# Performance work log

Measured on AMD Instinct MI355X. Metric: run time of the kernel, lower is better.

The kernel has to match this reference:

```python
import jax, jax.numpy as jnp
import numpy as np

B, S, HID = 1, 1024, 4096
NH, NKV, HD = 32, 8, 128
GROUPS = NH // NKV
THETA = 10000.0
SPAR = 0.5          # sparse_aggression (layer_idx > 0)
MIN_IDX = 4         # min_sparse_index: always-kept sink tokens
NEG = jnp.float32(-1e30)


def setup_inputs() -> dict:
    key = jax.random.key(0)
    k0, k1, k2, k3, k4 = jax.random.split(key, 5)
    sc = 0.02
    return {
        "hidden_states": jax.random.normal(k0, (B, S, HID), jnp.float32),
        "position_ids": jnp.arange(S, dtype=jnp.int32)[None, :],
        "Wq": jax.random.normal(k1, (NH * HD, HID), jnp.float32) * sc,
        "Wk": jax.random.normal(k2, (NKV * HD, HID), jnp.float32) * sc,
        "Wv": jax.random.normal(k3, (NKV * HD, HID), jnp.float32) * sc,
        "Wo": jax.random.normal(k4, (HID, NH * HD), jnp.float32) * sc,
    }


def _rotate_half(x):
    h = x.shape[-1] // 2
    return jnp.concatenate([-x[..., h:], x[..., :h]], axis=-1)


def _rope_cos_sin(position_ids):
    inv_freq = 1.0 / (THETA ** (jnp.arange(0, HD, 2, dtype=jnp.float32) / HD))
    freqs = position_ids.astype(jnp.float32)[..., None] * inv_freq  # [B,S,HD/2]
    emb = jnp.concatenate([freqs, freqs], axis=-1)                  # [B,S,HD]
    return jnp.cos(emb)[:, None], jnp.sin(emb)[:, None]             # [B,1,S,HD]


def reference(hidden_states, position_ids, Wq, Wk, Wv, Wo):
    b, s, _ = hidden_states.shape
    # QKV projections (nn.Linear: x @ W.T)
    q = (hidden_states @ Wq.T).reshape(b, s, NH, HD).transpose(0, 2, 1, 3)
    k = (hidden_states @ Wk.T).reshape(b, s, NKV, HD).transpose(0, 2, 1, 3)
    v = (hidden_states @ Wv.T).reshape(b, s, NKV, HD).transpose(0, 2, 1, 3)
    # RoPE
    cos, sin = _rope_cos_sin(position_ids)
    q = q * cos + _rotate_half(q) * sin
    k = k * cos + _rotate_half(k) * sin
    # repeat_kv (GQA expansion)
    k = jnp.repeat(k, GROUPS, axis=1)
    v = jnp.repeat(v, GROUPS, axis=1)
    # causal additive mask [1,1,S,S]
    causal = jnp.where(jnp.triu(jnp.ones((s, s), bool), 1), NEG, jnp.float32(0))[None, None]
    scale = 1.0 / np.sqrt(HD)
    scores = jnp.einsum('bhqd,bhkd->bhqk', q, k) * scale
    # oracle importance: softmax of (softmaxed) masked attention (no_grad in original)
    oracle = jax.nn.softmax((scores + causal).astype(jnp.float32), axis=-1)
    importance = jax.nn.softmax(oracle, axis=-1)
    importance = jax.lax.stop_gradient(importance)
    # descending sort -> rank of each key for each query
    sorted_idx = jnp.argsort(-importance, axis=-1)          # [B,H,S,S]
    ranks = jnp.argsort(sorted_idx, axis=-1)                # inverse perm
    # per-query token budget: keep ceil-ish top-k proportional to row length
    k_per_row = jnp.maximum((SPAR * (jnp.arange(s) + 1)).astype(jnp.int32), 1)
    key_idx = jnp.arange(s)
    kept = (ranks < k_per_row[None, None, :, None]) | (key_idx[None, None, None, :] < MIN_IDX)
    sparse_mask = jnp.where(kept, jnp.float32(0), NEG)
    # sparse attention
    attn = scores + sparse_mask + causal
    probs = jax.nn.softmax(attn.astype(jnp.float32), axis=-1).astype(v.dtype)
    out = jnp.einsum('bhqk,bhkd->bhqd', probs, v)           # [B,H,S,HD]
    out = out.transpose(0, 2, 1, 3).reshape(b, s, NH * HD)
    return out @ Wo.T
```

## Files before the change

### kernel.cpp

```cpp
#include <hip/hip_runtime.h>
#include <hip/hip_bf16.h>

#define S_LEN 1024
#define HID   4096
#define NH    32
#define NKV   8
#define HD    128
#define MIN_IDX 4
#define AO_COLS 4096
#define HEAD_STRIDE 131072

typedef __attribute__((ext_vector_type(8))) short short8;
typedef __attribute__((ext_vector_type(4))) float f32x4;

__device__ __forceinline__ unsigned short f2bf(float f) {
  union { float f; unsigned u; } v; v.f = f;
  unsigned r = v.u + 0x7FFFu + ((v.u >> 16) & 1u);
  return (unsigned short)(r >> 16);
}
__device__ __forceinline__ float bf2f(unsigned short h) {
  union { unsigned u; float f; } v; v.u = ((unsigned)h) << 16;
  return v.f;
}
__device__ __forceinline__ unsigned pk2(float a, float b) {
  union { __hip_bfloat162 h; unsigned u; } c;
  c.h = __float22bfloat162_rn(make_float2(a, b));
  return c.u;
}
__device__ __forceinline__ short8 pack8(float4 a, float4 b) {
  union { short8 s; unsigned u[4]; } r;
  r.u[0] = pk2(a.x, a.y); r.u[1] = pk2(a.z, a.w);
  r.u[2] = pk2(b.x, b.y); r.u[3] = pk2(b.z, b.w);
  return r.s;
}
__device__ __forceinline__ unsigned ordf(float f) {
  union { float f; int i; } v; v.f = f;
  return (unsigned)(v.i ^ ((v.i >> 31) | 0x80000000));
}
__device__ __forceinline__ float iordf(unsigned u) {
  union { int i; float f; } v;
  v.i = (u & 0x80000000u) ? (int)(u ^ 0x80000000u) : (int)~u;
  return v.f;
}
__device__ __forceinline__ float wave_sum_f(float v) {
  #pragma unroll
  for (int m = 32; m >= 1; m >>= 1) v += __shfl_xor(v, m);
  return v;
}
__device__ __forceinline__ unsigned wave_max_u(unsigned v) {
  #pragma unroll
  for (int m = 32; m >= 1; m >>= 1) { unsigned o = __shfl_xor(v, m); v = o > v ? o : v; }
  return v;
}
__device__ __forceinline__ void wave_lds_fence() {
  __builtin_amdgcn_s_waitcnt(0xC07F);
  __builtin_amdgcn_wave_barrier();
}
__device__ __forceinline__ void gload_lds16(const unsigned short* g, unsigned short* l) {
  auto gp = (const __attribute__((address_space(1))) unsigned*)g;
  auto lp = (__attribute__((address_space(3))) unsigned*)(unsigned)(unsigned long long)l;
  __builtin_amdgcn_global_load_lds(gp, lp, 16, 0, 0);
}

__global__ __launch_bounds__(256) void cvt_k(
    const float* __restrict__ src, unsigned short* __restrict__ dst)
{
  const size_t i = ((size_t)blockIdx.x * 256 + threadIdx.x) * 8;
  float4 a = *(const float4*)(src + i);
  float4 b = *(const float4*)(src + i + 4);
  *(short8*)(dst + i) = pack8(a, b);
}

__global__ __launch_bounds__(256) void cvt4_k(
    const float* __restrict__ s0, const float* __restrict__ s1,
    const float* __restrict__ s2, const float* __restrict__ s3,
    unsigned short* __restrict__ d0, unsigned short* __restrict__ d1)
{
  const int b = blockIdx.x;
  const float* src; unsigned short* dst; int rb;
  if (b < 2048)       { src = s0; dst = d0;            rb = b; }
  else if (b < 10240) { src = s1; dst = d1;            rb = b - 2048; }
  else if (b < 12288) { src = s2; dst = d1 + 16777216; rb = b - 10240; }
  else                { src = s3; dst = d1 + 20971520; rb = b - 12288; }
  const size_t i = ((size_t)rb * 256 + threadIdx.x) * 8;
  float4 a = *(const float4*)(src + i);
  float4 c = *(const float4*)(src + i + 4);
  *(short8*)(dst + i) = pack8(a, c);
}

__global__ __launch_bounds__(256) void gemm_qkv_k(
    const unsigned short* __restrict__ Xb, const unsigned short* __restrict__ Wb,
    unsigned short* __restrict__ Qraw, unsigned short* __restrict__ Kraw,
    unsigned short* __restrict__ Vt)
{
  __shared__ unsigned short As[3][128 * 32];
  __shared__ unsigned short Bs[3][128 * 32];
  const int nt = blockIdx.x;
  const int n0 = nt * 128;
  const int m0 = blockIdx.y * 128;
  const int t = threadIdx.x, w = t >> 6, lane = t & 63;
  const int wm = w >> 1, wn = w & 1;
  const int mcol = lane & 15, quad = lane >> 4;
  const int lrow = lane >> 2, lcol = (lane & 3) * 8;

  const unsigned short* Ag = Xb + (size_t)m0 * HID;
  const unsigned short* Bg = Wb + (size_t)n0 * HID;

  f32x4 acc[4][4];
  #pragma unroll
  for (int i = 0; i < 4; i++)
    #pragma unroll
    for (int j = 0; j < 4; j++) acc[i][j] = (f32x4){0.f, 0.f, 0.f, 0.f};

  constexpr int NT = HID / 32;
  #define STAGE_QKV(buf, k0)                                                  \
    { const int c0 = w * 2, c1 = w * 2 + 1;                                   \
      gload_lds16(Ag + (size_t)(c0*16 + lrow) * HID + (k0) + lcol, &As[buf][c0 * 512]); \
      gload_lds16(Bg + (size_t)(c0*16 + lrow) * HID + (k0) + lcol, &Bs[buf][c0 * 512]); \
      gload_lds16(Ag + (size_t)(c1*16 + lrow) * HID + (k0) + lcol, &As[buf][c1 * 512]); \
      gload_lds16(Bg + (size_t)(c1*16 + lrow) * HID + (k0) + lcol, &Bs[buf][c1 * 512]); }

  STAGE_QKV(0, 0)
  STAGE_QKV(1, 32)
  asm volatile("s_waitcnt vmcnt(4)" ::: "memory");
  __builtin_amdgcn_s_barrier();
  __builtin_amdgcn_sched_barrier(0);

  int cur = 0, stg = 2;
  for (int kt = 0; kt < NT; ++kt) {
    if (kt + 2 < NT) STAGE_QKV(stg, (kt + 2) * 32)
    short8 af[4], bf[4];
    #pragma unroll
    for (int i = 0; i < 4; i++) af[i] = *(const short8*)&As[cur][(wm*64 + i*16 + mcol)*32 + quad*8];
    #pragma unroll
    for (int j = 0; j < 4; j++) bf[j] = *(const short8*)&Bs[cur][(wn*64 + j*16 + mcol)*32 + quad*8];
    #pragma unroll
    for (int i = 0; i < 4; i++)
      #pragma unroll
      for (int j = 0; j < 4; j++)
        acc[i][j] = __builtin_amdgcn_mfma_f32_16x16x32_bf16(af[i], bf[j], acc[i][j], 0, 0, 0);
    if (kt + 2 < NT) { asm volatile("s_waitcnt vmcnt(4)" ::: "memory"); }
    else             { asm volatile("s_waitcnt vmcnt(0)" ::: "memory"); }
    __builtin_amdgcn_s_barrier();
    __builtin_amdgcn_sched_barrier(0);
    cur = (cur == 2) ? 0 : cur + 1;
    stg = (stg == 2) ? 0 : stg + 1;
  }

  if (nt < 40) {
    unsigned short* dst = (nt < 32) ? (Qraw + (size_t)nt * HEAD_STRIDE)
                                    : (Kraw + (size_t)(nt - 32) * HEAD_STRIDE);
    #pragma unroll
    for (int i = 0; i < 4; i++) {
      const int rb = m0 + wm*64 + i*16 + quad*4;
      #pragma unroll
      for (int j = 0; j < 4; j++) {
        const int d = wn*64 + j*16 + mcol;
        #pragma unroll
        for (int r = 0; r < 4; r++)
          dst[(size_t)(rb + r) * HD + d] = f2bf(acc[i][j][r]);
      }
    }
  } else {
    unsigned short* dst = Vt + (size_t)(nt - 40) * HEAD_STRIDE;
    #pragma unroll
    for (int i = 0; i < 4; i++) {
      const int rb = m0 + wm*64 + i*16 + quad*4;
      #pragma unroll
      for (int j = 0; j < 4; j++) {
        const int d = wn*64 + j*16 + mcol;
        ushort4 v4;
        v4.x = f2bf(acc[i][j][0]); v4.y = f2bf(acc[i][j][1]);
        v4.z = f2bf(acc[i][j][2]); v4.w = f2bf(acc[i][j][3]);
        *(ushort4*)(dst + (size_t)d * S_LEN + rb) = v4;
      }
    }
  }
}

__global__ __launch_bounds__(256) void rope_qk_k(
    const int* __restrict__ pos_ids,
    unsigned short* __restrict__ Qraw, unsigned short* __restrict__ Kraw)
{
  const int w = threadIdx.x >> 6, lane = threadIdx.x & 63;
  const int gw = blockIdx.x * 4 + w;
  const int hidx = gw >> 10;
  const int s = gw & 1023;
  const float pos = (float)pos_ids[s];
  const float invf = exp2f((float)lane * -0.20762050593045f);
  float sn, cs;
  sincosf(pos * invf, &sn, &cs);
  unsigned short* base = (hidx < NH)
      ? (Qraw + (size_t)hidx * HEAD_STRIDE + (size_t)s * HD)
      : (Kraw + (size_t)(hidx - NH) * HEAD_STRIDE + (size_t)s * HD);
  const float x0 = bf2f(base[lane]), x1 = bf2f(base[lane + 64]);
  base[lane]      = f2bf(x0 * cs - x1 * sn);
  base[lane + 64] = f2bf(x1 * cs + x0 * sn);
}

#define SROW 1042
#define PSTR 2084

#define PROC_ROW(UARR, RR, LL, PRE, PM, KRM, TTT)                             \
  {                                                                           \
    const int r_ = (RR);                                                      \
    const int L_ = (LL);                                                      \
    unsigned btau = (PRE);                                                    \
    unsigned bmsk = (PM);                                                     \
    int kr = (KRM);                                                           \
    int tt = (TTT);                                                           \
    const int bs = (bmsk == 0u) ? 31 : (__builtin_ctz(bmsk) - 1);             \
    _Pragma("unroll 1")                                                       \
    for (int b = bs; b >= 0; --b) {                                           \
      if (tt <= kr) break;                                                    \
      const unsigned bit = 1u << b;                                           \
      const unsigned am = bmsk | bit;                                         \
      const unsigned test = btau | bit;                                       \
      int cnt = 0;                                                            \
      _Pragma("unroll")                                                       \
      for (int c = 0; c < NC; c++) {                                          \
        const int j = c * 64 + lane;                                          \
        cnt += (int)__popcll(__ballot(j < L_ && ((UARR)[c] & am) == test));   \
      }                                                                       \
      if (cnt >= kr) { btau = test; tt = cnt; }                               \
      else           { kr -= cnt; tt -= cnt; }                                \
      bmsk = am;                                                              \
    }                                                                         \
    unsigned um = 0;                                                          \
    _Pragma("unroll")                                                         \
    for (int c = 0; c < NC; c++) {                                            \
      const int j = c * 64 + lane;                                            \
      if (j < L_ && (UARR)[c] > um) um = (UARR)[c];                           \
    }                                                                         \
    const float mx = iordf(wave_max_u(um));                                   \
    float ssum = 0.f;                                                         \
    int tiebase = 0;                                                          \
    _Pragma("unroll")                                                         \
    for (int c = 0; c < NC; c++) {                                            \
      const int j = c * 64 + lane;                                            \
      const unsigned u = (UARR)[c];                                           \
      const unsigned umv = u & bmsk;                                          \
      const bool eq = (j < L_) && (umv == btau);                              \
      const unsigned long long bal = __ballot(eq);                            \
      const int trank = tiebase + (int)__popcll(bal & lmlt);                  \
      tiebase += (int)__popcll(bal);                                          \
      const bool kept = (j < L_) &&                                           \
          ((umv > btau) || (eq && trank < kr) || (j < MIN_IDX));              \
      const float e = kept ? __expf(iordf(u) - mx) : 0.f;                     \
      Pl[r_][c*64 + lane] = f2bf(e);                                          \
      ssum += e;                                                              \
    }                                                                         \
    ssum = wave_sum_f(ssum);                                                  \
    if (lane == 0) rowinv[r_] = 1.f / fmaxf(ssum, 1e-30f);                    \
  }

template<int KT>
__device__ __forceinline__ void attn_body(
    const unsigned short* __restrict__ Qb, const unsigned short* __restrict__ Kh,
    const unsigned short* __restrict__ Vh, unsigned short* __restrict__ AO,
    float (*S)[SROW], unsigned (*hist)[256], float* rowinv,
    int q0, int h, int w, int lane, int mcol, int quad)
{
  constexpr int NC = 2 * KT;
  const float scale = 0.08838834764831845f;
  unsigned short (*Pl)[PSTR] = (unsigned short (*)[PSTR])&S[0][0];
  const int wk = w & 3, wp = w >> 2;

  short8 aq[4];
  {
    const unsigned short* qrow = Qb + ((size_t)h * S_LEN + q0 + mcol) * HD + quad * 8;
    #pragma unroll
    for (int kk = 0; kk < 4; kk++) aq[kk] = *(const short8*)(qrow + kk * 32);
  }

  #pragma unroll
  for (int kt = wp; kt < KT; kt += 2) {
    short8 bfr[2][4];
    #pragma unroll
    for (int g2 = 0; g2 < 2; g2++) {
      const int key = kt * 128 + (wk * 2 + g2) * 16 + mcol;
      const unsigned short* krow = Kh + (size_t)key * HD + quad * 8;
      #pragma unroll
      for (int kk = 0; kk < 4; kk++) bfr[g2][kk] = *(const short8*)(krow + kk * 32);
    }
    f32x4 d4[2];
    d4[0] = (f32x4){0.f,0.f,0.f,0.f}; d4[1] = (f32x4){0.f,0.f,0.f,0.f};
    #pragma unroll
    for (int g2 = 0; g2 < 2; g2++)
      #pragma unroll
      for (int kk = 0; kk < 4; kk++)
        d4[g2] = __builtin_amdgcn_mfma_f32_16x16x32_bf16(aq[kk], bfr[g2][kk], d4[g2], 0, 0, 0);
    #pragma unroll
    for (int g2 = 0; g2 < 2; g2++) {
      const int ckey = kt * 128 + (wk * 2 + g2) * 16 + mcol;
      #pragma unroll
      for (int r = 0; r < 4; r++) S[quad*4 + r][ckey] = d4[g2][r] * scale;
    }
  }
  __syncthreads();

  const unsigned long long lmlt = (1ull << lane) - 1ull;
  const int rep = lane & 3;
  {
    const int ra = w * 2, rbn = ra + 1;
    const int L0 = q0 + ra + 1, L1 = q0 + rbn + 1;
    unsigned u0[NC], u1[NC];
    #pragma unroll
    for (int c = 0; c < NC; c++) {
      u0[c] = ordf(S[ra][c*64 + lane]);
      u1[c] = ordf(S[rbn][c*64 + lane]);
    }
    int ks0 = L0 >> 1; if (ks0 < 1) ks0 = 1;
    int ks1 = L1 >> 1; if (ks1 < 1) ks1 = 1;
    int krem0 = ks0, tot0 = L0, krem1 = ks1, tot1 = L1;
    unsigned pre0 = 0u, pre1 = 0u, pm0 = 0u, pm1 = 0u;

    #pragma unroll
    for (int pass = 0; pass < 3; pass++) {
      const int shift = 26 - pass * 6;
      const bool a0 = tot0 > krem0, a1 = tot1 > krem1;
      if (!a0 && !a1) continue;
      { uint4 z = {0u, 0u, 0u, 0u}; *(uint4*)&hist[w][lane * 4] = z; }
      wave_lds_fence();
      #pragma unroll
      for (int c = 0; c < NC; c++) {
        const int j = c * 64 + lane;
        if (a0 && j < L0 && (u0[c] & pm0) == pre0)
          atomicAdd(&hist[w][((u0[c] >> shift) & 63) * 4 + rep], 1u);
        if (a1 && j < L1 && (u1[c] & pm1) == pre1)
          atomicAdd(&hist[w][((u1[c] >> shift) & 63) * 4 + rep], 1u << 16);
      }
      wave_lds_fence();
      const uint4 cv = *(const uint4*)&hist[w][(63 - lane) * 4];
      const unsigned cnt2 = cv.x + cv.y + cv.z + cv.w;
      unsigned x = cnt2;
      #pragma unroll
      for (int d2 = 1; d2 < 64; d2 <<= 1) { unsigned y = __shfl_up(x, d2); if (lane >= d2) x += y; }
      const unsigned runp = x - cnt2;
      if (a0) {
        const int run = (int)(runp & 0xFFFFu);
        const int cn  = (int)(cnt2 & 0xFFFFu);
        const bool hit = (run < krem0) && (run + cn >= krem0);
        unsigned packv = hit ? (((unsigned)(63 - lane) << 22) |
                                ((unsigned)run << 11) | (unsigned)cn) : 0u;
        const unsigned long long bal = __ballot(hit);
        const int srcl = __ffsll(bal) - 1;
        const unsigned res = __shfl(packv, srcl);
        krem0 -= (int)((res >> 11) & 0x7FF);
        tot0 = (int)(res & 0x7FF);
        pre0 |= ((unsigned)(res >> 22)) << shift;
        pm0 |= 63u << shift;
      }
      if (a1) {
        const int run = (int)(runp >> 16);
        const int cn  = (int)(cnt2 >> 16);
        const bool hit = (run < krem1) && (run + cn >= krem1);
        unsigned packv = hit ? (((unsigned)(63 - lane) << 22) |
                                ((unsigned)run << 11) | (unsigned)cn) : 0u;
        const unsigned long long bal = __ballot(hit);
        const int srcl = __ffsll(bal) - 1;
        const unsigned res = __shfl(packv, srcl);
        krem1 -= (int)((res >> 11) & 0x7FF);
        tot1 = (int)(res & 0x7FF);
        pre1 |= ((unsigned)(res >> 22)) << shift;
        pm1 |= 63u << shift;
      }
    }
    PROC_ROW(u0, ra,  L0, pre0, pm0, krem0, tot0)
    PROC_ROW(u1, rbn, L1, pre1, pm1, krem1, tot1)
  }
  __syncthreads();

  f32x4 opv = (f32x4){0.f,0.f,0.f,0.f};
  const int d = w * 16 + mcol;
  #pragma unroll
  for (int kt = 0; kt < KT; kt++) {
    #pragma unroll
    for (int kb = 0; kb < 4; kb++) {
      short8 af = *(const short8*)&Pl[mcol][kt*128 + kb*32 + quad*8];
      short8 bfr = *(const short8*)(Vh + (size_t)d * S_LEN + kt*128 + kb*32 + quad*8);
      opv = __builtin_amdgcn_mfma_f32_16x16x32_bf16(af, bfr, opv, 0, 0, 0);
    }
  }
  {
    const int col = h * HD + d;
    #pragma unroll
    for (int r2 = 0; r2 < 4; r2++) {
      const int row = q0 + quad*4 + r2;
      AO[(size_t)row * AO_COLS + col] = f2bf(opv[r2] * rowinv[quad*4 + r2]);
    }
  }
}

__global__ __launch_bounds__(512, 4) void attn_k(
    const unsigned short* __restrict__ Qb, const unsigned short* __restrict__ Kb,
    const unsigned short* __restrict__ Vt, unsigned short* __restrict__ AO)
{
  __shared__ float S[16][SROW];
  __shared__ unsigned hist[8][256];
  __shared__ float rowinv[16];
  const int rb = (int)gridDim.x - 1 - (int)blockIdx.x;
  const int h = blockIdx.y;
  const int kvh = h >> 2;
  const int q0 = rb * 16;
  const int kt_max = (rb >> 3) + 1;
  const int t = threadIdx.x, w = t >> 6, lane = t & 63;
  const int mcol = lane & 15, quad = lane >> 4;
  const unsigned short* Kh = Kb + (size_t)kvh * HEAD_STRIDE;
  const unsigned short* Vh = Vt + (size_t)kvh * HEAD_STRIDE;

  switch (kt_max) {
    case 1: attn_body<1>(Qb, Kh, Vh, AO, S, hist, rowinv, q0, h, w, lane, mcol, quad); break;
    case 2: attn_body<2>(Qb, Kh, Vh, AO, S, hist, rowinv, q0, h, w, lane, mcol, quad); break;
    case 3: attn_body<3>(Qb, Kh, Vh, AO, S, hist, rowinv, q0, h, w, lane, mcol, quad); break;
    case 4: attn_body<4>(Qb, Kh, Vh, AO, S, hist, rowinv, q0, h, w, lane, mcol, quad); break;
    case 5: attn_body<5>(Qb, Kh, Vh, AO, S, hist, rowinv, q0, h, w, lane, mcol, quad); break;
    case 6: attn_body<6>(Qb, Kh, Vh, AO, S, hist, rowinv, q0, h, w, lane, mcol, quad); break;
    case 7: attn_body<7>(Qb, Kh, Vh, AO, S, hist, rowinv, q0, h, w, lane, mcol, quad); break;
    default: attn_body<8>(Qb, Kh, Vh, AO, S, hist, rowinv, q0, h, w, lane, mcol, quad); break;
  }
}

__global__ __launch_bounds__(256) void gemm_out_k(
    const unsigned short* __restrict__ A, const unsigned short* __restrict__ Wob,
    float* __restrict__ Out)
{
  __shared__ unsigned short As[3][128 * 32];
  __shared__ unsigned short Bs[3][128 * 32];
  const int n0 = blockIdx.x * 128;
  const int m0 = blockIdx.y * 128;
  const int t = threadIdx.x, w = t >> 6, lane = t & 63;
  const int wm = w >> 1, wn = w & 1;
  const int mcol = lane & 15, quad = lane >> 4;
  const int lrow = lane >> 2, lcol = (lane & 3) * 8;

  const unsigned short* Ag = A   + (size_t)m0 * AO_COLS;
  const unsigned short* Bg = Wob + (size_t)n0 * AO_COLS;

  f32x4 acc[4][4];
  #pragma unroll
  for (int i = 0; i < 4; i++)
    #pragma unroll
    for (int j = 0; j < 4; j++) acc[i][j] = (f32x4){0.f, 0.f, 0.f, 0.f};

  constexpr int NT = AO_COLS / 32;
  #define STAGE_OUT(buf, k0)                                                  \
    { const int c0 = w * 2, c1 = w * 2 + 1;                                   \
      gload_lds16(Ag + (size_t)(c0*16 + lrow) * AO_COLS + (k0) + lcol, &As[buf][c0 * 512]); \
      gload_lds16(Bg + (size_t)(c0*16 + lrow) * AO_COLS + (k0) + lcol, &Bs[buf][c0 * 512]); \
      gload_lds16(Ag + (size_t)(c1*16 + lrow) * AO_COLS + (k0) + lcol, &As[buf][c1 * 512]); \
      gload_lds16(Bg + (size_t)(c1*16 + lrow) * AO_COLS + (k0) + lcol, &Bs[buf][c1 * 512]); }

  STAGE_OUT(0, 0)
  STAGE_OUT(1, 32)
  asm volatile("s_waitcnt vmcnt(4)" ::: "memory");
  __builtin_amdgcn_s_barrier();
  __builtin_amdgcn_sched_barrier(0);

  int cur = 0, stg = 2;
  for (int kt = 0; kt < NT; ++kt) {
    if (kt + 2 < NT) STAGE_OUT(stg, (kt + 2) * 32)
    short8 af[4], bf[4];
    #pragma unroll
    for (int i = 0; i < 4; i++) af[i] = *(const short8*)&As[cur][(wm*64 + i*16 + mcol)*32 + quad*8];
    #pragma unroll
    for (int j = 0; j < 4; j++) bf[j] = *(const short8*)&Bs[cur][(wn*64 + j*16 + mcol)*32 + quad*8];
    #pragma unroll
    for (int i = 0; i < 4; i++)
      #pragma unroll
      for (int j = 0; j < 4; j++)
        acc[i][j] = __builtin_amdgcn_mfma_f32_16x16x32_bf16(af[i], bf[j], acc[i][j], 0, 0, 0);
    if (kt + 2 < NT) { asm volatile("s_waitcnt vmcnt(4)" ::: "memory"); }
    else             { asm volatile("s_waitcnt vmcnt(0)" ::: "memory"); }
    __builtin_amdgcn_s_barrier();
    __builtin_amdgcn_sched_barrier(0);
    cur = (cur == 2) ? 0 : cur + 1;
    stg = (stg == 2) ? 0 : stg + 1;
  }

  #pragma unroll
  for (int i = 0; i < 4; i++) {
    const int rb = m0 + wm*64 + i*16 + quad*4;
    #pragma unroll
    for (int j = 0; j < 4; j++) {
      const int col = n0 + wn*64 + j*16 + mcol;
      #pragma unroll
      for (int r = 0; r < 4; r++)
        Out[(size_t)(rb + r) * HID + col] = acc[i][j][r];
    }
  }
}

extern "C" void kernel_launch(void* const* d_in, const int* in_sizes, int n_in,
                              void* d_out, int out_size, void* d_ws, size_t ws_size,
                              hipStream_t stream) {
  (void)in_sizes; (void)n_in; (void)out_size; (void)ws_size;
  const float* X   = (const float*)d_in[0];
  const int*   pos = (const int*)d_in[1];
  const float* Wq  = (const float*)d_in[2];
  const float* Wk  = (const float*)d_in[3];
  const float* Wv  = (const float*)d_in[4];
  const float* Wo  = (const float*)d_in[5];
  float* out = (float*)d_out;

  char* ws = (char*)d_ws;
  unsigned short* Qraw  = (unsigned short*)ws;
  unsigned short* Kraw  = (unsigned short*)(ws + 8388608);
  unsigned short* Vt    = (unsigned short*)(ws + 10485760);
  unsigned short* AO    = (unsigned short*)(ws + 12582912);
  unsigned short* Xb    = (unsigned short*)(ws + 20971520);
  unsigned short* Wqkvb = (unsigned short*)(ws + 29360128);
  unsigned short* Wob   = Wqkvb;

  cvt4_k<<<dim3(14336), dim3(256), 0, stream>>>(X, Wq, Wk, Wv, Xb, Wqkvb);

  gemm_qkv_k<<<dim3(48, 8),  dim3(256), 0, stream>>>(Xb, Wqkvb, Qraw, Kraw, Vt);
  rope_qk_k <<<dim3(10240),  dim3(256), 0, stream>>>(pos, Qraw, Kraw);

  cvt_k<<<dim3(8192), dim3(256), 0, stream>>>(Wo, Wob);

  attn_k    <<<dim3(64, 32), dim3(512), 0, stream>>>(Qraw, Kraw, Vt, AO);
  gemm_out_k<<<dim3(32, 8),  dim3(256), 0, stream>>>(AO, Wob, out);
}
```

Baseline: 462.7 us.

## Halve GEMM N-tiles for better CU fill and add tie-free fast path in top-k

Both the QKV and output-projection GEMMs move from 128x128 to 128x64 tiles, doubling the block count, with per-kernel launch-bound occupancy hints and fewer B-tile loads per stage. The QKV kernel now treats Q and K as one contiguous buffer, so the separate K pointer is dropped from it and from RoPE. The attention top-k masking gains a fast path that skips tie ranking with ballots whenever the threshold bucket holds no more keys than are still needed. The aim is better occupancy across the GPU's compute units for the GEMMs and fewer wave-wide reductions in the sparse softmax. The cost is less data reuse per tile in the GEMMs.

```diff
diff --git a/kernel.cpp b/kernel.cpp
--- a/kernel.cpp
+++ b/kernel.cpp
@@ -88,15 +88,14 @@
   *(short8*)(dst + i) = pack8(a, c);
 }
 
-__global__ __launch_bounds__(256) void gemm_qkv_k(
+__global__ __launch_bounds__(256, 3) void gemm_qkv_k(
     const unsigned short* __restrict__ Xb, const unsigned short* __restrict__ Wb,
-    unsigned short* __restrict__ Qraw, unsigned short* __restrict__ Kraw,
-    unsigned short* __restrict__ Vt)
+    unsigned short* __restrict__ Qraw, unsigned short* __restrict__ Vt)
 {
   __shared__ unsigned short As[3][128 * 32];
-  __shared__ unsigned short Bs[3][128 * 32];
+  __shared__ unsigned short Bs[3][64 * 32];
   const int nt = blockIdx.x;
-  const int n0 = nt * 128;
+  const int n0 = nt * 64;
   const int m0 = blockIdx.y * 128;
   const int t = threadIdx.x, w = t >> 6, lane = t & 63;
   const int wm = w >> 1, wn = w & 1;
@@ -106,40 +105,39 @@
   const unsigned short* Ag = Xb + (size_t)m0 * HID;
   const unsigned short* Bg = Wb + (size_t)n0 * HID;
 
-  f32x4 acc[4][4];
+  f32x4 acc[4][2];
   #pragma unroll
   for (int i = 0; i < 4; i++)
     #pragma unroll
-    for (int j = 0; j < 4; j++) acc[i][j] = (f32x4){0.f, 0.f, 0.f, 0.f};
+    for (int j = 0; j < 2; j++) acc[i][j] = (f32x4){0.f, 0.f, 0.f, 0.f};
 
   constexpr int NT = HID / 32;
   #define STAGE_QKV(buf, k0)                                                  \
     { const int c0 = w * 2, c1 = w * 2 + 1;                                   \
       gload_lds16(Ag + (size_t)(c0*16 + lrow) * HID + (k0) + lcol, &As[buf][c0 * 512]); \
-      gload_lds16(Bg + (size_t)(c0*16 + lrow) * HID + (k0) + lcol, &Bs[buf][c0 * 512]); \
       gload_lds16(Ag + (size_t)(c1*16 + lrow) * HID + (k0) + lcol, &As[buf][c1 * 512]); \
-      gload_lds16(Bg + (size_t)(c1*16 + lrow) * HID + (k0) + lcol, &Bs[buf][c1 * 512]); }
+      gload_lds16(Bg + (size_t)(w*16 + lrow) * HID + (k0) + lcol, &Bs[buf][w * 512]); }
 
   STAGE_QKV(0, 0)
   STAGE_QKV(1, 32)
-  asm volatile("s_waitcnt vmcnt(4)" ::: "memory");
+  asm volatile("s_waitcnt vmcnt(3)" ::: "memory");
   __builtin_amdgcn_s_barrier();
   __builtin_amdgcn_sched_barrier(0);
 
   int cur = 0, stg = 2;
   for (int kt = 0; kt < NT; ++kt) {
     if (kt + 2 < NT) STAGE_QKV(stg, (kt + 2) * 32)
-    short8 af[4], bf[4];
+    short8 af[4], bfr[2];
     #pragma unroll
     for (int i = 0; i < 4; i++) af[i] = *(const short8*)&As[cur][(wm*64 + i*16 + mcol)*32 + quad*8];
     #pragma unroll
-    for (int j = 0; j < 4; j++) bf[j] = *(const short8*)&Bs[cur][(wn*64 + j*16 + mcol)*32 + quad*8];
+    for (int j = 0; j < 2; j++) bfr[j] = *(const short8*)&Bs[cur][(wn*32 + j*16 + mcol)*32 + quad*8];
     #pragma unroll
     for (int i = 0; i < 4; i++)
       #pragma unroll
-      for (int j = 0; j < 4; j++)
-        acc[i][j] = __builtin_amdgcn_mfma_f32_16x16x32_bf16(af[i], bf[j], acc[i][j], 0, 0, 0);
-    if (kt + 2 < NT) { asm volatile("s_waitcnt vmcnt(4)" ::: "memory"); }
+      for (int j = 0; j < 2; j++)
+        acc[i][j] = __builtin_amdgcn_mfma_f32_16x16x32_bf16(af[i], bfr[j], acc[i][j], 0, 0, 0);
+    if (kt + 2 < NT) { asm volatile("s_waitcnt vmcnt(3)" ::: "memory"); }
     else             { asm volatile("s_waitcnt vmcnt(0)" ::: "memory"); }
     __builtin_amdgcn_s_barrier();
     __builtin_amdgcn_sched_barrier(0);
@@ -147,28 +145,30 @@
     stg = (stg == 2) ? 0 : stg + 1;
   }
 
-  if (nt < 40) {
-    unsigned short* dst = (nt < 32) ? (Qraw + (size_t)nt * HEAD_STRIDE)
-                                    : (Kraw + (size_t)(nt - 32) * HEAD_STRIDE);
+  if (nt < 80) {
+    unsigned short* dst = Qraw + (size_t)(n0 >> 7) * HEAD_STRIDE;
+    const int cb = n0 & 127;
     #pragma unroll
     for (int i = 0; i < 4; i++) {
       const int rb = m0 + wm*64 + i*16 + quad*4;
       #pragma unroll
-      for (int j = 0; j < 4; j++) {
-        const int d = wn*64 + j*16 + mcol;
+      for (int j = 0; j < 2; j++) {
+        const int d = cb + wn*32 + j*16 + mcol;
         #pragma unroll
         for (int r = 0; r < 4; r++)
           dst[(size_t)(rb + r) * HD + d] = f2bf(acc[i][j][r]);
       }
     }
   } else {
-    unsigned short* dst = Vt + (size_t)(nt - 40) * HEAD_STRIDE;
+    const int v0 = n0 - 5120;
+    unsigned short* dst = Vt + (size_t)(v0 >> 7) * HEAD_STRIDE;
+    const int cb = v0 & 127;
     #pragma unroll
     for (int i = 0; i < 4; i++) {
       const int rb = m0 + wm*64 + i*16 + quad*4;
       #pragma unroll
-      for (int j = 0; j < 4; j++) {
-        const int d = wn*64 + j*16 + mcol;
+      for (int j = 0; j < 2; j++) {
+        const int d = cb + wn*32 + j*16 + mcol;
         ushort4 v4;
         v4.x = f2bf(acc[i][j][0]); v4.y = f2bf(acc[i][j][1]);
         v4.z = f2bf(acc[i][j][2]); v4.w = f2bf(acc[i][j][3]);
@@ -179,8 +179,7 @@
 }
 
 __global__ __launch_bounds__(256) void rope_qk_k(
-    const int* __restrict__ pos_ids,
-    unsigned short* __restrict__ Qraw, unsigned short* __restrict__ Kraw)
+    const int* __restrict__ pos_ids, unsigned short* __restrict__ Qraw)
 {
   const int w = threadIdx.x >> 6, lane = threadIdx.x & 63;
   const int gw = blockIdx.x * 4 + w;
@@ -190,9 +189,7 @@
   const float invf = exp2f((float)lane * -0.20762050593045f);
   float sn, cs;
   sincosf(pos * invf, &sn, &cs);
-  unsigned short* base = (hidx < NH)
-      ? (Qraw + (size_t)hidx * HEAD_STRIDE + (size_t)s * HD)
-      : (Kraw + (size_t)(hidx - NH) * HEAD_STRIDE + (size_t)s * HD);
+  unsigned short* base = Qraw + (size_t)hidx * HEAD_STRIDE + (size_t)s * HD;
   const float x0 = bf2f(base[lane]), x1 = bf2f(base[lane + 64]);
   base[lane]      = f2bf(x0 * cs - x1 * sn);
   base[lane + 64] = f2bf(x1 * cs + x0 * sn);
@@ -234,21 +231,34 @@
     }                                                                         \
     const float mx = iordf(wave_max_u(um));                                   \
     float ssum = 0.f;                                                         \
-    int tiebase = 0;                                                          \
-    _Pragma("unroll")                                                         \
-    for (int c = 0; c < NC; c++) {                                            \
-      const int j = c * 64 + lane;                                            \
-      const unsigned u = (UARR)[c];                                           \
-      const unsigned umv = u & bmsk;                                          \
-      const bool eq = (j < L_) && (umv == btau);                              \
-      const unsigned long long bal = __ballot(eq);                            \
-      const int trank = tiebase + (int)__popcll(bal & lmlt);                  \
-      tiebase += (int)__popcll(bal);                                          \
-      const bool kept = (j < L_) &&                                           \
-          ((umv > btau) || (eq && trank < kr) || (j < MIN_IDX));              \
-      const float e = kept ? __expf(iordf(u) - mx) : 0.f;                     \
-      Pl[r_][c*64 + lane] = f2bf(e);                                          \
-      ssum += e;                                                              \
+    if (tt <= kr) {                                                           \
+           \
+      _Pragma("unroll")                                                       \
+      for (int c = 0; c < NC; c++) {                                          \
+        const int j = c * 64 + lane;                                          \
+        const unsigned u = (UARR)[c];                                         \
+        const bool kept = (j < L_) && ((u >= btau) || (j < MIN_IDX));         \
+        const float e = kept ? __expf(iordf(u) - mx) : 0.f;                   \
+        Pl[r_][c*64 + lane] = f2bf(e);                                        \
+        ssum += e;                                                            \
+      }                                                                       \
+    } else {                                                                  \
+      int tiebase = 0;                                                        \
+      _Pragma("unroll")                                                       \
+      for (int c = 0; c < NC; c++) {                                          \
+        const int j = c * 64 + lane;                                          \
+        const unsigned u = (UARR)[c];                                         \
+        const unsigned umv = u & bmsk;                                        \
+        const bool eq = (j < L_) && (umv == btau);                            \
+        const unsigned long long bal = __ballot(eq);                          \
+        const int trank = tiebase + (int)__popcll(bal & lmlt);                \
+        tiebase += (int)__popcll(bal);                                        \
+        const bool kept = (j < L_) &&                                         \
+            ((umv > btau) || (eq && trank < kr) || (j < MIN_IDX));            \
+        const float e = kept ? __expf(iordf(u) - mx) : 0.f;                   \
+        Pl[r_][c*64 + lane] = f2bf(e);                                        \
+        ssum += e;                                                            \
+      }                                                                       \
     }                                                                         \
     ssum = wave_sum_f(ssum);                                                  \
     if (lane == 0) rowinv[r_] = 1.f / fmaxf(ssum, 1e-30f);                    \
@@ -421,13 +431,13 @@
   }
 }
 
-__global__ __launch_bounds__(256) void gemm_out_k(
+__global__ __launch_bounds__(256, 2) void gemm_out_k(
     const unsigned short* __restrict__ A, const unsigned short* __restrict__ Wob,
     float* __restrict__ Out)
 {
   __shared__ unsigned short As[3][128 * 32];
-  __shared__ unsigned short Bs[3][128 * 32];
-  const int n0 = blockIdx.x * 128;
+  __shared__ unsigned short Bs[3][64 * 32];
+  const int n0 = blockIdx.x * 64;
   const int m0 = blockIdx.y * 128;
   const int t = threadIdx.x, w = t >> 6, lane = t & 63;
   const int wm = w >> 1, wn = w & 1;
@@ -437,40 +447,39 @@
   const unsigned short* Ag = A   + (size_t)m0 * AO_COLS;
   const unsigned short* Bg = Wob + (size_t)n0 * AO_COLS;
 
-  f32x4 acc[4][4];
+  f32x4 acc[4][2];
   #pragma unroll
   for (int i = 0; i < 4; i++)
     #pragma unroll
-    for (int j = 0; j < 4; j++) acc[i][j] = (f32x4){0.f, 0.f, 0.f, 0.f};
+    for (int j = 0; j < 2; j++) acc[i][j] = (f32x4){0.f, 0.f, 0.f, 0.f};
 
   constexpr int NT = AO_COLS / 32;
   #define STAGE_OUT(buf, k0)                                                  \
     { const int c0 = w * 2, c1 = w * 2 + 1;                                   \
       gload_lds16(Ag + (size_t)(c0*16 + lrow) * AO_COLS + (k0) + lcol, &As[buf][c0 * 512]); \
-      gload_lds16(Bg + (size_t)(c0*16 + lrow) * AO_COLS + (k0) + lcol, &Bs[buf][c0 * 512]); \
       gload_lds16(Ag + (size_t)(c1*16 + lrow) * AO_COLS + (k0) + lcol, &As[buf][c1 * 512]); \
-      gload_lds16(Bg + (size_t)(c1*16 + lrow) * AO_COLS + (k0) + lcol, &Bs[buf][c1 * 512]); }
+      gload_lds16(Bg + (size_t)(w*16 + lrow) * AO_COLS + (k0) + lcol, &Bs[buf][w * 512]); }
 
   STAGE_OUT(0, 0)
   STAGE_OUT(1, 32)
-  asm volatile("s_waitcnt vmcnt(4)" ::: "memory");
+  asm volatile("s_waitcnt vmcnt(3)" ::: "memory");
   __builtin_amdgcn_s_barrier();
   __builtin_amdgcn_sched_barrier(0);
 
   int cur = 0, stg = 2;
   for (int kt = 0; kt < NT; ++kt) {
     if (kt + 2 < NT) STAGE_OUT(stg, (kt + 2) * 32)
-    short8 af[4], bf[4];
+    short8 af[4], bfr[2];
     #pragma unroll
     for (int i = 0; i < 4; i++) af[i] = *(const short8*)&As[cur][(wm*64 + i*16 + mcol)*32 + quad*8];
     #pragma unroll
-    for (int j = 0; j < 4; j++) bf[j] = *(const short8*)&Bs[cur][(wn*64 + j*16 + mcol)*32 + quad*8];
+    for (int j = 0; j < 2; j++) bfr[j] = *(const short8*)&Bs[cur][(wn*32 + j*16 + mcol)*32 + quad*8];
     #pragma unroll
     for (int i = 0; i < 4; i++)
       #pragma unroll
-      for (int j = 0; j < 4; j++)
-        acc[i][j] = __builtin_amdgcn_mfma_f32_16x16x32_bf16(af[i], bf[j], acc[i][j], 0, 0, 0);
-    if (kt + 2 < NT) { asm volatile("s_waitcnt vmcnt(4)" ::: "memory"); }
+      for (int j = 0; j < 2; j++)
+        acc[i][j] = __builtin_amdgcn_mfma_f32_16x16x32_bf16(af[i], bfr[j], acc[i][j], 0, 0, 0);
+    if (kt + 2 < NT) { asm volatile("s_waitcnt vmcnt(3)" ::: "memory"); }
     else             { asm volatile("s_waitcnt vmcnt(0)" ::: "memory"); }
     __builtin_amdgcn_s_barrier();
     __builtin_amdgcn_sched_barrier(0);
@@ -482,8 +491,8 @@
   for (int i = 0; i < 4; i++) {
     const int rb = m0 + wm*64 + i*16 + quad*4;
     #pragma unroll
-    for (int j = 0; j < 4; j++) {
-      const int col = n0 + wn*64 + j*16 + mcol;
+    for (int j = 0; j < 2; j++) {
+      const int col = n0 + wn*32 + j*16 + mcol;
       #pragma unroll
       for (int r = 0; r < 4; r++)
         Out[(size_t)(rb + r) * HID + col] = acc[i][j][r];
@@ -514,11 +523,11 @@
 
   cvt4_k<<<dim3(14336), dim3(256), 0, stream>>>(X, Wq, Wk, Wv, Xb, Wqkvb);
 
-  gemm_qkv_k<<<dim3(48, 8),  dim3(256), 0, stream>>>(Xb, Wqkvb, Qraw, Kraw, Vt);
-  rope_qk_k <<<dim3(10240),  dim3(256), 0, stream>>>(pos, Qraw, Kraw);
+  gemm_qkv_k<<<dim3(96, 8),  dim3(256), 0, stream>>>(Xb, Wqkvb, Qraw, Vt);
+  rope_qk_k <<<dim3(10240),  dim3(256), 0, stream>>>(pos, Qraw);
 
   cvt_k<<<dim3(8192), dim3(256), 0, stream>>>(Wo, Wob);
 
   attn_k    <<<dim3(64, 32), dim3(512), 0, stream>>>(Qraw, Kraw, Vt, AO);
-  gemm_out_k<<<dim3(32, 8),  dim3(256), 0, stream>>>(AO, Wob, out);
-}
+  gemm_out_k<<<dim3(64, 8),  dim3(256), 0, stream>>>(AO, Wob, out);
+}
```

After: 475.6 us. 1.03x slower.

## Fuse Wo conversion into attention, split-K output GEMM, fast-path tie-free rows

Applied to the files above, without the earlier changes.

The standalone Wo fp32-to-bf16 conversion kernel is folded into extra blocks at the end of the attention grid, and the grid is flattened to one dimension. The output projection becomes a two-way split-K GEMM that accumulates with atomicAdd into an output cleared by a memset, so twice as many blocks are available to fill the CUs. The sparse top-k masking gets a fast path for rows where all tied keys are kept, which skips the ballot and popcount tie ranking. Q and K are now addressed as one contiguous buffer. In exchange there is an extra memset, float atomics that make the output summation order nondeterministic, and extra work in the attention launch.

```diff
diff --git a/kernel.cpp b/kernel.cpp
--- a/kernel.cpp
+++ b/kernel.cpp
@@ -60,15 +60,6 @@
   auto gp = (const __attribute__((address_space(1))) unsigned*)g;
   auto lp = (__attribute__((address_space(3))) unsigned*)(unsigned)(unsigned long long)l;
   __builtin_amdgcn_global_load_lds(gp, lp, 16, 0, 0);
-}
-
-__global__ __launch_bounds__(256) void cvt_k(
-    const float* __restrict__ src, unsigned short* __restrict__ dst)
-{
-  const size_t i = ((size_t)blockIdx.x * 256 + threadIdx.x) * 8;
-  float4 a = *(const float4*)(src + i);
-  float4 b = *(const float4*)(src + i + 4);
-  *(short8*)(dst + i) = pack8(a, b);
 }
 
 __global__ __launch_bounds__(256) void cvt4_k(
@@ -90,8 +81,7 @@
 
 __global__ __launch_bounds__(256) void gemm_qkv_k(
     const unsigned short* __restrict__ Xb, const unsigned short* __restrict__ Wb,
-    unsigned short* __restrict__ Qraw, unsigned short* __restrict__ Kraw,
-    unsigned short* __restrict__ Vt)
+    unsigned short* __restrict__ Qraw, unsigned short* __restrict__ Vt)
 {
   __shared__ unsigned short As[3][128 * 32];
   __shared__ unsigned short Bs[3][128 * 32];
@@ -148,8 +138,7 @@
   }
 
   if (nt < 40) {
-    unsigned short* dst = (nt < 32) ? (Qraw + (size_t)nt * HEAD_STRIDE)
-                                    : (Kraw + (size_t)(nt - 32) * HEAD_STRIDE);
+    unsigned short* dst = Qraw + (size_t)nt * HEAD_STRIDE;
     #pragma unroll
     for (int i = 0; i < 4; i++) {
       const int rb = m0 + wm*64 + i*16 + quad*4;
@@ -179,8 +168,7 @@
 }
 
 __global__ __launch_bounds__(256) void rope_qk_k(
-    const int* __restrict__ pos_ids,
-    unsigned short* __restrict__ Qraw, unsigned short* __restrict__ Kraw)
+    const int* __restrict__ pos_ids, unsigned short* __restrict__ Qraw)
 {
   const int w = threadIdx.x >> 6, lane = threadIdx.x & 63;
   const int gw = blockIdx.x * 4 + w;
@@ -190,9 +178,7 @@
   const float invf = exp2f((float)lane * -0.20762050593045f);
   float sn, cs;
   sincosf(pos * invf, &sn, &cs);
-  unsigned short* base = (hidx < NH)
-      ? (Qraw + (size_t)hidx * HEAD_STRIDE + (size_t)s * HD)
-      : (Kraw + (size_t)(hidx - NH) * HEAD_STRIDE + (size_t)s * HD);
+  unsigned short* base = Qraw + (size_t)hidx * HEAD_STRIDE + (size_t)s * HD;
   const float x0 = bf2f(base[lane]), x1 = bf2f(base[lane + 64]);
   base[lane]      = f2bf(x0 * cs - x1 * sn);
   base[lane + 64] = f2bf(x1 * cs + x0 * sn);
@@ -234,21 +220,34 @@
     }                                                                         \
     const float mx = iordf(wave_max_u(um));                                   \
     float ssum = 0.f;                                                         \
-    int tiebase = 0;                                                          \
-    _Pragma("unroll")                                                         \
-    for (int c = 0; c < NC; c++) {                                            \
-      const int j = c * 64 + lane;                                            \
-      const unsigned u = (UARR)[c];                                           \
-      const unsigned umv = u & bmsk;                                          \
-      const bool eq = (j < L_) && (umv == btau);                              \
-      const unsigned long long bal = __ballot(eq);                            \
-      const int trank = tiebase + (int)__popcll(bal & lmlt);                  \
-      tiebase += (int)__popcll(bal);                                          \
-      const bool kept = (j < L_) &&                                           \
-          ((umv > btau) || (eq && trank < kr) || (j < MIN_IDX));              \
-      const float e = kept ? __expf(iordf(u) - mx) : 0.f;                     \
-      Pl[r_][c*64 + lane] = f2bf(e);                                          \
-      ssum += e;                                                              \
+    if (tt <= kr) {                                                           \
+           \
+      _Pragma("unroll")                                                       \
+      for (int c = 0; c < NC; c++) {                                          \
+        const int j = c * 64 + lane;                                          \
+        const unsigned u = (UARR)[c];                                         \
+        const bool kept = (j < L_) && ((u >= btau) || (j < MIN_IDX));         \
+        const float e = kept ? __expf(iordf(u) - mx) : 0.f;                   \
+        Pl[r_][c*64 + lane] = f2bf(e);                                        \
+        ssum += e;                                                            \
+      }                                                                       \
+    } else {                                                                  \
+      int tiebase = 0;                                                        \
+      _Pragma("unroll")                                                       \
+      for (int c = 0; c < NC; c++) {                                          \
+        const int j = c * 64 + lane;                                          \
+        const unsigned u = (UARR)[c];                                         \
+        const unsigned umv = u & bmsk;                                        \
+        const bool eq = (j < L_) && (umv == btau);                            \
+        const unsigned long long bal = __ballot(eq);                          \
+        const int trank = tiebase + (int)__popcll(bal & lmlt);                \
+        tiebase += (int)__popcll(bal);                                        \
+        const bool kept = (j < L_) &&                                         \
+            ((umv > btau) || (eq && trank < kr) || (j < MIN_IDX));            \
+        const float e = kept ? __expf(iordf(u) - mx) : 0.f;                   \
+        Pl[r_][c*64 + lane] = f2bf(e);                                        \
+        ssum += e;                                                            \
+      }                                                                       \
     }                                                                         \
     ssum = wave_sum_f(ssum);                                                  \
     if (lane == 0) rowinv[r_] = 1.f / fmaxf(ssum, 1e-30f);                    \
@@ -394,13 +393,23 @@
 
 __global__ __launch_bounds__(512, 4) void attn_k(
     const unsigned short* __restrict__ Qb, const unsigned short* __restrict__ Kb,
-    const unsigned short* __restrict__ Vt, unsigned short* __restrict__ AO)
+    const unsigned short* __restrict__ Vt, unsigned short* __restrict__ AO,
+    const float* __restrict__ WoF, unsigned short* __restrict__ Wob)
 {
   __shared__ float S[16][SROW];
   __shared__ unsigned hist[8][256];
   __shared__ float rowinv[16];
-  const int rb = (int)gridDim.x - 1 - (int)blockIdx.x;
-  const int h = blockIdx.y;
+  const int bid = (int)blockIdx.x;
+  if (bid >= 2048) {
+    const size_t i = ((size_t)(bid - 2048) * 512 + threadIdx.x) * 8;
+    float4 a = *(const float4*)(WoF + i);
+    float4 c = *(const float4*)(WoF + i + 4);
+    *(short8*)(Wob + i) = pack8(a, c);
+    return;
+  }
+  const int bx = bid & 63;
+  const int h = bid >> 6;
+  const int rb = 63 - bx;
   const int kvh = h >> 2;
   const int q0 = rb * 16;
   const int kt_max = (rb >> 3) + 1;
@@ -429,13 +438,14 @@
   __shared__ unsigned short Bs[3][128 * 32];
   const int n0 = blockIdx.x * 128;
   const int m0 = blockIdx.y * 128;
+  const int kbase = blockIdx.z * 2048;
   const int t = threadIdx.x, w = t >> 6, lane = t & 63;
   const int wm = w >> 1, wn = w & 1;
   const int mcol = lane & 15, quad = lane >> 4;
   const int lrow = lane >> 2, lcol = (lane & 3) * 8;
 
-  const unsigned short* Ag = A   + (size_t)m0 * AO_COLS;
-  const unsigned short* Bg = Wob + (size_t)n0 * AO_COLS;
+  const unsigned short* Ag = A   + (size_t)m0 * AO_COLS + kbase;
+  const unsigned short* Bg = Wob + (size_t)n0 * AO_COLS + kbase;
 
   f32x4 acc[4][4];
   #pragma unroll
@@ -443,7 +453,7 @@
     #pragma unroll
     for (int j = 0; j < 4; j++) acc[i][j] = (f32x4){0.f, 0.f, 0.f, 0.f};
 
-  constexpr int NT = AO_COLS / 32;
+  constexpr int NT = 2048 / 32;
   #define STAGE_OUT(buf, k0)                                                  \
     { const int c0 = w * 2, c1 = w * 2 + 1;                                   \
       gload_lds16(Ag + (size_t)(c0*16 + lrow) * AO_COLS + (k0) + lcol, &As[buf][c0 * 512]); \
@@ -486,7 +496,7 @@
       const int col = n0 + wn*64 + j*16 + mcol;
       #pragma unroll
       for (int r = 0; r < 4; r++)
-        Out[(size_t)(rb + r) * HID + col] = acc[i][j][r];
+        atomicAdd(&Out[(size_t)(rb + r) * HID + col], acc[i][j][r]);
     }
   }
 }
@@ -514,11 +524,11 @@
 
   cvt4_k<<<dim3(14336), dim3(256), 0, stream>>>(X, Wq, Wk, Wv, Xb, Wqkvb);
 
-  gemm_qkv_k<<<dim3(48, 8),  dim3(256), 0, stream>>>(Xb, Wqkvb, Qraw, Kraw, Vt);
-  rope_qk_k <<<dim3(10240),  dim3(256), 0, stream>>>(pos, Qraw, Kraw);
-
-  cvt_k<<<dim3(8192), dim3(256), 0, stream>>>(Wo, Wob);
-
-  attn_k    <<<dim3(64, 32), dim3(512), 0, stream>>>(Qraw, Kraw, Vt, AO);
-  gemm_out_k<<<dim3(32, 8),  dim3(256), 0, stream>>>(AO, Wob, out);
-}
+  gemm_qkv_k<<<dim3(48, 8),  dim3(256), 0, stream>>>(Xb, Wqkvb, Qraw, Vt);
+  rope_qk_k <<<dim3(10240),  dim3(256), 0, stream>>>(pos, Qraw);
+
+  hipMemsetAsync(out, 0, (size_t)S_LEN * HID * sizeof(float), stream);
+
+  attn_k    <<<dim3(6144),   dim3(512), 0, stream>>>(Qraw, Kraw, Vt, AO, Wo, Wob);
+  gemm_out_k<<<dim3(32, 8, 2), dim3(256), 0, stream>>>(AO, Wob, out);
+}
```

New measurement: 446.6 us (median of 2 runs). 3.5% less time.
